# Kernel tuning notes

Measured on AMD Instinct MI355X. Metric: run time of the kernel, lower is better.

Reference implementation:

```python
import jax, jax.numpy as jnp
import numpy as np
from jax import lax

DIM = 512


def rmsnorm(x, gamma):
    # F.normalize(x, dim=-1) * sqrt(dim) * (gamma + 1)
    n = jnp.maximum(jnp.linalg.norm(x, axis=-1, keepdims=True), 1e-12)
    return x / n * (DIM ** 0.5) * (gamma + 1.0)


def lru_layer(x, Wn, Wif, Whf, bhf):
    # x: [b, t, d]. Precompute the input-dependent projections as big matmuls,
    # then scan the genuinely sequential hidden recurrence.
    nh = jnp.tanh(jnp.einsum('btd,de->bte', x, Wn))   # candidate hidden
    ifg = jnp.einsum('btd,de->bte', x, Wif)            # input forget logits
    b = x.shape[0]
    h0 = jnp.zeros((b, DIM), dtype=x.dtype)            # init_hidden buffer (zeros)

    def step(h, inp):
        nh_t, if_t = inp                               # [b, d] each
        g = jax.nn.sigmoid(h @ Whf + bhf + if_t)       # forget gate
        h_next = h + g * (nh_t - h)                    # lerp(h, nh, g)
        return h_next, h_next

    _, hs = lax.scan(step, h0, (jnp.swapaxes(nh, 0, 1), jnp.swapaxes(ifg, 0, 1)))
    return jnp.swapaxes(hs, 0, 1)                      # [b, t, d]


def gate_cell(x, hidden, Wn, Wif, Whf, bhf):
    # LightRecurrentUnitCell applied pointwise over [b, t, d] with hidden=x_in
    nh = jnp.tanh(jnp.einsum('btd,de->bte', x, Wn))
    g = jax.nn.sigmoid(jnp.einsum('btd,de->bte', hidden, Whf) + bhf
                       + jnp.einsum('btd,de->bte', x, Wif))
    return hidden + g * (nh - hidden)


def setup_inputs() -> dict:
    key = jax.random.key(0)
    ks = jax.random.split(key, 12)
    s = 1.0 / np.sqrt(DIM)
    def w(k):
        return jax.random.uniform(k, (DIM, DIM), jnp.float32, -s, s)
    inp = {
        'x': jax.random.normal(ks[0], (32, 2048, DIM), jnp.float32),
        'gamma': jnp.zeros((DIM,), jnp.float32),
        'g_Wn': w(ks[1]), 'g_Wif': w(ks[2]), 'g_Whf': w(ks[3]),
        'g_bhf': jax.random.uniform(ks[4], (DIM,), jnp.float32, -s, s),
        'l0_Wn': w(ks[5]), 'l0_Wif': w(ks[6]), 'l0_Whf': w(ks[7]),
        'l0_bhf': jax.random.uniform(ks[8], (DIM,), jnp.float32, -s, s),
        'l1_Wn': w(ks[9]), 'l1_Wif': w(ks[10]), 'l1_Whf': w(ks[11]),
        'l1_bhf': jax.random.uniform(jax.random.fold_in(key, 99), (DIM,), jnp.float32, -s, s),
    }
    return inp


def reference(x, gamma, g_Wn, g_Wif, g_Whf, g_bhf,
              l0_Wn, l0_Wif, l0_Whf, l0_bhf,
              l1_Wn, l1_Wif, l1_Whf, l1_bhf):
    xn = rmsnorm(x, gamma)
    h = lru_layer(xn, l0_Wn, l0_Wif, l0_Whf, l0_bhf)
    h = lru_layer(h, l1_Wn, l1_Wif, l1_Whf, l1_bhf)
    lru_out = gate_cell(h, xn, g_Wn, g_Wif, g_Whf, g_bhf)
    return lru_out + x
```

## Files before the change

kernel.cpp:

```cpp
#include <hip/hip_runtime.h>
#include <stdint.h>

#define D 512
#define BATCH 32
#define TT 2048
#define BT (BATCH*TT)

typedef unsigned short u16;
typedef __attribute__((ext_vector_type(8))) short bf16x8;
typedef __attribute__((ext_vector_type(4))) float f32x4;

__device__ __forceinline__ float bf2f(u16 u){
  union { unsigned int i; float f; } v; v.i = ((unsigned int)u) << 16; return v.f;
}
__device__ __forceinline__ u16 f2bf(float f){
  union { float f; unsigned int i; } v; v.f = f;
  unsigned int r = (v.i + 0x7fffu + ((v.i >> 16) & 1u)) >> 16;
  return (u16)r;
}

__device__ __forceinline__ int dot4i8(int a, int b, int c){
#if __has_builtin(__builtin_amdgcn_sdot4)
  return __builtin_amdgcn_sdot4(a, b, c, false);
#else
  c += (int)(char)(a      ) * (int)(char)(b      );
  c += (int)(char)(a >>  8) * (int)(char)(b >>  8);
  c += (int)(char)(a >> 16) * (int)(char)(b >> 16);
  c += (int)(char)(a >> 24) * (int)(char)(b >> 24);
  return c;
#endif
}

__global__ __launch_bounds__(256) void rmsnorm_k(const float* __restrict__ x,
                                                 const float* __restrict__ gamma,
                                                 u16* __restrict__ xn){
  int row = blockIdx.x;
  int t = threadIdx.x;
  const float* xr = x + (size_t)row * D;
  float v0 = xr[t];
  float v1 = xr[t + 256];
  float s = v0*v0 + v1*v1;
  #pragma unroll
  for (int o = 32; o > 0; o >>= 1) s += __shfl_down(s, o);
  __shared__ float red[4];
  int lane = t & 63, wv = t >> 6;
  if (lane == 0) red[wv] = s;
  __syncthreads();
  float tot = red[0] + red[1] + red[2] + red[3];
  float n = fmaxf(sqrtf(tot), 1e-12f);
  float sc = 22.627416997969522f / n;
  u16* o_ = xn + (size_t)row * D;
  o_[t]       = f2bf(v0 * sc * (gamma[t] + 1.f));
  o_[t + 256] = f2bf(v1 * sc * (gamma[t + 256] + 1.f));
}

__global__ __launch_bounds__(256) void transpose_k(const float* __restrict__ src,
                                                   u16* __restrict__ dst){
  __shared__ u16 tile[32][33];
  int bx = blockIdx.x * 32, by = blockIdx.y * 32;
  int tx = threadIdx.x & 31, ty = threadIdx.x >> 5;
  #pragma unroll
  for (int i = 0; i < 32; i += 8)
    tile[ty + i][tx] = f2bf(src[(size_t)(by + ty + i) * D + bx + tx]);
  __syncthreads();
  #pragma unroll
  for (int i = 0; i < 32; i += 8)
    dst[(size_t)(bx + ty + i) * D + by + tx] = tile[tx][ty + i];
}

__global__ __launch_bounds__(64) void quant_col_k(const float* __restrict__ W,
                                                  int* __restrict__ Wq,
                                                  float* __restrict__ sc){
  int e = blockIdx.x;
  int lane = threadIdx.x;
  float w[8];
  float m = 0.f;
  #pragma unroll
  for (int j = 0; j < 8; j++){
    w[j] = W[(size_t)(lane*8 + j) * D + e];
    m = fmaxf(m, fabsf(w[j]));
  }
  #pragma unroll
  for (int o = 32; o > 0; o >>= 1) m = fmaxf(m, __shfl_xor(m, o));
  float inv = (m > 0.f) ? (127.f / m) : 0.f;
  int q[8];
  #pragma unroll
  for (int j = 0; j < 8; j++){
    int v = __float2int_rn(w[j] * inv);
    v = v < -127 ? -127 : (v > 127 ? 127 : v);
    q[j] = v & 0xff;
  }
  int p0 = q[0] | (q[1] << 8) | (q[2] << 16) | (q[3] << 24);
  int p1 = q[4] | (q[5] << 8) | (q[6] << 16) | (q[7] << 24);
  Wq[e*128 + lane*2]     = p0;
  Wq[e*128 + lane*2 + 1] = p1;
  if (lane == 0) sc[e] = m / (127.f * 127.f);
}

__global__ __launch_bounds__(256) void gemm_bt_k(const u16* __restrict__ A,
                                                 const u16* __restrict__ Bt,
                                                 u16* __restrict__ C,
                                                 int do_tanh){
  __shared__ __align__(16) u16 As[128*32];
  __shared__ __align__(16) u16 Bs[128*32];
  int tid = threadIdx.x;
  int bm = blockIdx.x, bn = blockIdx.y;
  int wv = tid >> 6, lane = tid & 63;
  int wm = (wv & 1) * 64, wn = (wv >> 1) * 64;
  int m0 = lane & 15, quad = lane >> 4;
  f32x4 acc[4][4];
  #pragma unroll
  for (int i = 0; i < 4; i++)
    #pragma unroll
    for (int j = 0; j < 4; j++){
      f32x4 z = {0.f, 0.f, 0.f, 0.f};
      acc[i][j] = z;
    }
  const size_t arow = (size_t)bm * 128;
  const size_t brow = (size_t)bn * 128;
  for (int k0 = 0; k0 < D; k0 += 32){
    __syncthreads();
    #pragma unroll
    for (int i = 0; i < 2; i++){
      int c = tid + 256*i;
      int r = c >> 2, ko = (c & 3) * 8;
      ((int4*)As)[c] = *(const int4*)(A  + (arow + r) * D + k0 + ko);
      ((int4*)Bs)[c] = *(const int4*)(Bt + (brow + r) * D + k0 + ko);
    }
    __syncthreads();
    bf16x8 af[4], bfr[4];
    #pragma unroll
    for (int i = 0; i < 4; i++){
      af[i]  = *(const bf16x8*)(As + (wm + i*16 + m0) * 32 + quad*8);
      bfr[i] = *(const bf16x8*)(Bs + (wn + i*16 + m0) * 32 + quad*8);
    }
    #pragma unroll
    for (int i = 0; i < 4; i++)
      #pragma unroll
      for (int j = 0; j < 4; j++)
        acc[i][j] = __builtin_amdgcn_mfma_f32_16x16x32_bf16(af[i], bfr[j], acc[i][j], 0, 0, 0);
  }
  #pragma unroll
  for (int i = 0; i < 4; i++)
    #pragma unroll
    for (int j = 0; j < 4; j++)
      #pragma unroll
      for (int r = 0; r < 4; r++){
        size_t row = arow + wm + i*16 + quad*4 + r;
        int col = bn*128 + wn + j*16 + m0;
        float v = acc[i][j][r];
        if (do_tanh) v = tanhf(v);
        C[row * D + col] = f2bf(v);
      }
}

__global__ __launch_bounds__(512, 2) void lru_scan_k(u16* __restrict__ Nn,
                                                     const u16* __restrict__ Ff,
                                                     const int* __restrict__ Wq,
                                                     const float* __restrict__ sc,
                                                     const float* __restrict__ bhf){
  int e = threadIdx.x;
  int b = blockIdx.x;
  int w[128];
  #pragma unroll
  for (int i = 0; i < 128; i++) w[i] = Wq[e*128 + i];
  float scale = sc[e];
  float bias  = bhf[e];
  __shared__ __align__(16) int hq[2][128];
  if (e < 128) hq[0][e] = 0;
  float h = 0.f;
  const size_t base = (size_t)b * TT * D + e;
  u16* np = Nn + base;
  const u16* fp = Ff + base;
  float nv = bf2f(np[0]);
  float fv = bf2f(fp[0]);
  __syncthreads();
  for (int t = 0; t < TT; t++){
    float nv_n = 0.f, fv_n = 0.f;
    if (t < TT - 1){
      nv_n = bf2f(np[(size_t)(t+1) * D]);
      fv_n = bf2f(fp[(size_t)(t+1) * D]);
    }
    const int* hb = hq[t & 1];
    int z = 0;
    #pragma unroll
    for (int i = 0; i < 32; i++){
      int4 hc = ((const int4*)hb)[i];
      z = dot4i8(w[4*i+0], hc.x, z);
      z = dot4i8(w[4*i+1], hc.y, z);
      z = dot4i8(w[4*i+2], hc.z, z);
      z = dot4i8(w[4*i+3], hc.w, z);
    }
    float arg = (float)z * scale + bias + fv;
    float g = 1.f / (1.f + __expf(-arg));
    h = h + g * (nv - h);
    np[(size_t)t * D] = f2bf(h);
    int q = __float2int_rn(h * 127.f);
    q = q < -127 ? -127 : (q > 127 ? 127 : q);
    ((char*)hq[(t+1) & 1])[e] = (char)q;
    nv = nv_n; fv = fv_n;
    __syncthreads();
  }
}

__global__ __launch_bounds__(256) void final1_k(const u16* __restrict__ xn,
                                                u16* __restrict__ Nng,
                                                const u16* __restrict__ Ffg,
                                                const u16* __restrict__ Ghf,
                                                const float* __restrict__ gbhf){
  size_t i = (size_t)blockIdx.x * 256 + threadIdx.x;
  int e = (int)(i & (D - 1));
  float xnv = bf2f(xn[i]);
  float nv  = bf2f(Nng[i]);
  float arg = bf2f(Ghf[i]) + gbhf[e] + bf2f(Ffg[i]);
  float g = 1.f / (1.f + __expf(-arg));
  float lru = xnv + g * (nv - xnv);
  Nng[i] = f2bf(lru);
}

__global__ __launch_bounds__(256) void final2_k(const u16* __restrict__ lru,
                                                const float* __restrict__ x,
                                                float* __restrict__ out){
  size_t i = (size_t)blockIdx.x * 256 + threadIdx.x;
  out[i] = bf2f(lru[i]) + x[i];
}

extern "C" void kernel_launch(void* const* d_in, const int* in_sizes, int n_in,
                              void* d_out, int out_size, void* d_ws, size_t ws_size,
                              hipStream_t stream){
  const float* x      = (const float*)d_in[0];
  const float* gamma  = (const float*)d_in[1];
  const float* g_Wn   = (const float*)d_in[2];
  const float* g_Wif  = (const float*)d_in[3];
  const float* g_Whf  = (const float*)d_in[4];
  const float* g_bhf  = (const float*)d_in[5];
  const float* l0_Wn  = (const float*)d_in[6];
  const float* l0_Wif = (const float*)d_in[7];
  const float* l0_Whf = (const float*)d_in[8];
  const float* l0_bhf = (const float*)d_in[9];
  const float* l1_Wn  = (const float*)d_in[10];
  const float* l1_Wif = (const float*)d_in[11];
  const float* l1_Whf = (const float*)d_in[12];
  const float* l1_bhf = (const float*)d_in[13];
  float* out = (float*)d_out;

  char* ws = (char*)d_ws;
  const size_t PLANE = (size_t)BT * D * 2;
  u16* P0 = (u16*)(ws);
  u16* P1 = (u16*)(ws + PLANE);
  u16* P2 = (u16*)d_out;
  u16* P3 = P2 + (size_t)BT * D;

  char* wb = ws + 2*PLANE;
  const size_t WSZ = (size_t)D * D * 2;
  u16* T_l0Wn  = (u16*)(wb + 0*WSZ);
  u16* T_l0Wif = (u16*)(wb + 1*WSZ);
  u16* T_gWhf  = (u16*)(wb + 2*WSZ);
  u16* T_l1Wn  = (u16*)(wb + 3*WSZ);
  u16* T_l1Wif = (u16*)(wb + 4*WSZ);
  u16* T_gWn   = (u16*)(wb + 5*WSZ);
  u16* T_gWif  = (u16*)(wb + 6*WSZ);
  int*   Wq0 = (int*)  (wb + 7*WSZ);
  int*   Wq1 = (int*)  (wb + 7*WSZ + (size_t)D*D);
  float* sc0 = (float*)(wb + 7*WSZ + 2*(size_t)D*D);
  float* sc1 = (float*)(wb + 7*WSZ + 2*(size_t)D*D + D*4);

  dim3 tb(256), tg(16, 16);
  transpose_k<<<tg, tb, 0, stream>>>(l0_Wn,  T_l0Wn);
  transpose_k<<<tg, tb, 0, stream>>>(l0_Wif, T_l0Wif);
  transpose_k<<<tg, tb, 0, stream>>>(g_Whf,  T_gWhf);
  transpose_k<<<tg, tb, 0, stream>>>(l1_Wn,  T_l1Wn);
  transpose_k<<<tg, tb, 0, stream>>>(l1_Wif, T_l1Wif);
  transpose_k<<<tg, tb, 0, stream>>>(g_Wn,   T_gWn);
  transpose_k<<<tg, tb, 0, stream>>>(g_Wif,  T_gWif);
  quant_col_k<<<512, 64, 0, stream>>>(l0_Whf, Wq0, sc0);
  quant_col_k<<<512, 64, 0, stream>>>(l1_Whf, Wq1, sc1);

  rmsnorm_k<<<BT, 256, 0, stream>>>(x, gamma, P0);

  dim3 gg(BT/128, D/128);
  gemm_bt_k<<<gg, tb, 0, stream>>>(P0, T_l0Wn,  P1, 1);
  gemm_bt_k<<<gg, tb, 0, stream>>>(P0, T_l0Wif, P2, 0);
  lru_scan_k<<<BATCH, 512, 0, stream>>>(P1, P2, Wq0, sc0, l0_bhf);
  gemm_bt_k<<<gg, tb, 0, stream>>>(P1, T_l1Wn,  P3, 1);
  gemm_bt_k<<<gg, tb, 0, stream>>>(P1, T_l1Wif, P2, 0);
  lru_scan_k<<<BATCH, 512, 0, stream>>>(P3, P2, Wq1, sc1, l1_bhf);
  gemm_bt_k<<<gg, tb, 0, stream>>>(P3, T_gWn,  P1, 1);
  gemm_bt_k<<<gg, tb, 0, stream>>>(P3, T_gWif, P2, 0);
  gemm_bt_k<<<gg, tb, 0, stream>>>(P0, T_gWhf, P3, 0);

  final1_k<<<BT*D/256, 256, 0, stream>>>(P0, P1, P2, P3, g_bhf);
  final2_k<<<BT*D/256, 256, 0, stream>>>(P1, x, out);
}
```

Baseline: 4.231 ms.

## Split scan dot product between LDS reads and readlane broadcasts with four accumulators

In the LRU scan kernel, each thread now reads the first half of the quantized hidden vector from shared memory as before. For the second half it loads one word per lane and broadcasts it with readlane, which moves part of the traffic off LDS onto scalar registers. The dot product is split across four independent accumulators to shorten the dependency chain, and the bias is folded into the prefetched forget-gate value. Launch bounds drop to one block per SM to leave room for registers. This lowers occupancy, which may hide less latency across batches.

```diff
diff --git a/kernel.cpp b/kernel.cpp
--- a/kernel.cpp
+++ b/kernel.cpp
@@ -28,6 +28,14 @@
   c += (int)(char)(a >> 16) * (int)(char)(b >> 16);
   c += (int)(char)(a >> 24) * (int)(char)(b >> 24);
   return c;
+#endif
+}
+
+__device__ __forceinline__ int rdlane(int v, int l){
+#if __has_builtin(__builtin_amdgcn_readlane)
+  return __builtin_amdgcn_readlane(v, l);
+#else
+  return __shfl(v, l);
 #endif
 }
 
@@ -154,16 +162,19 @@
       }
 }
 
-__global__ __launch_bounds__(512, 2) void lru_scan_k(u16* __restrict__ Nn,
+__global__ __launch_bounds__(512, 1) void lru_scan_k(u16* __restrict__ Nn,
                                                      const u16* __restrict__ Ff,
                                                      const int* __restrict__ Wq,
                                                      const float* __restrict__ sc,
                                                      const float* __restrict__ bhf){
   int e = threadIdx.x;
   int b = blockIdx.x;
-  int w[128];
-  #pragma unroll
-  for (int i = 0; i < 128; i++) w[i] = Wq[e*128 + i];
+  int lane64 = e & 63;
+  int w[64], w2[64];
+  #pragma unroll
+  for (int i = 0; i < 64; i++) w[i]  = Wq[e*128 + i];
+  #pragma unroll
+  for (int i = 0; i < 64; i++) w2[i] = Wq[e*128 + 64 + i];
   float scale = sc[e];
   float bias  = bhf[e];
   __shared__ __align__(16) int hq[2][128];
@@ -172,33 +183,40 @@
   const size_t base = (size_t)b * TT * D + e;
   u16* np = Nn + base;
   const u16* fp = Ff + base;
-  float nv = bf2f(np[0]);
-  float fv = bf2f(fp[0]);
+  float nv  = bf2f(np[0]);
+  float fvb = bf2f(fp[0]) + bias;
   __syncthreads();
   for (int t = 0; t < TT; t++){
-    float nv_n = 0.f, fv_n = 0.f;
+    float nv_n = 0.f, fvb_n = 0.f;
     if (t < TT - 1){
-      nv_n = bf2f(np[(size_t)(t+1) * D]);
-      fv_n = bf2f(fp[(size_t)(t+1) * D]);
+      nv_n  = bf2f(np[(size_t)(t+1) * D]);
+      fvb_n = bf2f(fp[(size_t)(t+1) * D]) + bias;
     }
     const int* hb = hq[t & 1];
-    int z = 0;
-    #pragma unroll
-    for (int i = 0; i < 32; i++){
+    int hrl = hb[64 + lane64];
+    int zz[4] = {0, 0, 0, 0};
+    #pragma unroll
+    for (int i = 0; i < 16; i++){
       int4 hc = ((const int4*)hb)[i];
-      z = dot4i8(w[4*i+0], hc.x, z);
-      z = dot4i8(w[4*i+1], hc.y, z);
-      z = dot4i8(w[4*i+2], hc.z, z);
-      z = dot4i8(w[4*i+3], hc.w, z);
-    }
-    float arg = (float)z * scale + bias + fv;
+      zz[0] = dot4i8(w[4*i+0], hc.x, zz[0]);
+      zz[1] = dot4i8(w[4*i+1], hc.y, zz[1]);
+      zz[2] = dot4i8(w[4*i+2], hc.z, zz[2]);
+      zz[3] = dot4i8(w[4*i+3], hc.w, zz[3]);
+    }
+    #pragma unroll
+    for (int m = 0; m < 64; m++){
+      int s = rdlane(hrl, m);
+      zz[m & 3] = dot4i8(w2[m], s, zz[m & 3]);
+    }
+    int z = (zz[0] + zz[1]) + (zz[2] + zz[3]);
+    float arg = (float)z * scale + fvb;
     float g = 1.f / (1.f + __expf(-arg));
     h = h + g * (nv - h);
     np[(size_t)t * D] = f2bf(h);
     int q = __float2int_rn(h * 127.f);
     q = q < -127 ? -127 : (q > 127 ? 127 : q);
     ((char*)hq[(t+1) & 1])[e] = (char)q;
-    nv = nv_n; fv = fv_n;
+    nv = nv_n; fvb = fvb_n;
     __syncthreads();
   }
 }
```

New measurement: 4.696 ms. +11.0%, slower.

## Use int8 MFMA for the recurrent matvec in the LRU scan kernel

Applied to the files above, without the earlier changes.

Replaces the per-thread sdot4 loop over 128 packed weight registers with 16x16x64 int8 MFMA instructions. Each wave holds its 64 output columns as B fragments and broadcasts the quantized hidden state as the A operand. Only row 0 of each accumulator is used, so most of the MFMA work is wasted, but the per-thread dependent dot chain becomes a few matrix ops. It also folds the bias into the prefetched forget-gate input and swaps __syncthreads for a raw waitcnt plus s_barrier.

```diff
diff --git a/kernel.cpp b/kernel.cpp
--- a/kernel.cpp
+++ b/kernel.cpp
@@ -9,6 +9,7 @@
 typedef unsigned short u16;
 typedef __attribute__((ext_vector_type(8))) short bf16x8;
 typedef __attribute__((ext_vector_type(4))) float f32x4;
+typedef __attribute__((ext_vector_type(4))) int i32x4;
 
 __device__ __forceinline__ float bf2f(u16 u){
   union { unsigned int i; float f; } v; v.i = ((unsigned int)u) << 16; return v.f;
@@ -17,18 +18,6 @@
   union { float f; unsigned int i; } v; v.f = f;
   unsigned int r = (v.i + 0x7fffu + ((v.i >> 16) & 1u)) >> 16;
   return (u16)r;
-}
-
-__device__ __forceinline__ int dot4i8(int a, int b, int c){
-#if __has_builtin(__builtin_amdgcn_sdot4)
-  return __builtin_amdgcn_sdot4(a, b, c, false);
-#else
-  c += (int)(char)(a      ) * (int)(char)(b      );
-  c += (int)(char)(a >>  8) * (int)(char)(b >>  8);
-  c += (int)(char)(a >> 16) * (int)(char)(b >> 16);
-  c += (int)(char)(a >> 24) * (int)(char)(b >> 24);
-  return c;
-#endif
 }
 
 __global__ __launch_bounds__(256) void rmsnorm_k(const float* __restrict__ x,
@@ -159,47 +148,61 @@
                                                      const int* __restrict__ Wq,
                                                      const float* __restrict__ sc,
                                                      const float* __restrict__ bhf){
-  int e = threadIdx.x;
+  int tid = threadIdx.x;
   int b = blockIdx.x;
-  int w[128];
-  #pragma unroll
-  for (int i = 0; i < 128; i++) w[i] = Wq[e*128 + i];
+  int wv  = tid >> 6;
+  int l   = tid & 63;
+  int grp = l >> 4;
+  int col = l & 15;
+  int e   = wv * 64 + l;
+
+  i32x4 bf[4][8];
+  #pragma unroll
+  for (int j = 0; j < 4; j++){
+    const int* wp = Wq + (wv*64 + j*16 + col) * 128;
+    #pragma unroll
+    for (int c = 0; c < 8; c++)
+      bf[j][c] = *(const i32x4*)(wp + c*16 + grp*4);
+  }
   float scale = sc[e];
   float bias  = bhf[e];
-  __shared__ __align__(16) int hq[2][128];
-  if (e < 128) hq[0][e] = 0;
+
+  __shared__ __align__(16) char hq[2][512];
+  if (tid < 128) ((int*)hq[0])[tid] = 0;
   float h = 0.f;
   const size_t base = (size_t)b * TT * D + e;
   u16* np = Nn + base;
   const u16* fp = Ff + base;
-  float nv = bf2f(np[0]);
-  float fv = bf2f(fp[0]);
+  float nv  = bf2f(np[0]);
+  float fvb = bf2f(fp[0]) + bias;
   __syncthreads();
+
   for (int t = 0; t < TT; t++){
-    float nv_n = 0.f, fv_n = 0.f;
+    float nv_n = 0.f, fvb_n = 0.f;
     if (t < TT - 1){
-      nv_n = bf2f(np[(size_t)(t+1) * D]);
-      fv_n = bf2f(fp[(size_t)(t+1) * D]);
-    }
-    const int* hb = hq[t & 1];
-    int z = 0;
-    #pragma unroll
-    for (int i = 0; i < 32; i++){
-      int4 hc = ((const int4*)hb)[i];
-      z = dot4i8(w[4*i+0], hc.x, z);
-      z = dot4i8(w[4*i+1], hc.y, z);
-      z = dot4i8(w[4*i+2], hc.z, z);
-      z = dot4i8(w[4*i+3], hc.w, z);
-    }
-    float arg = (float)z * scale + bias + fv;
+      nv_n  = bf2f(np[(size_t)(t+1) * D]);
+      fvb_n = bf2f(fp[(size_t)(t+1) * D]) + bias;
+    }
+    const char* hb = hq[t & 1];
+    i32x4 acc0 = {0,0,0,0}, acc1 = {0,0,0,0}, acc2 = {0,0,0,0}, acc3 = {0,0,0,0};
+    #pragma unroll
+    for (int c = 0; c < 8; c++){
+      i32x4 a = *(const i32x4*)(hb + c*64 + grp*16);
+      acc0 = __builtin_amdgcn_mfma_i32_16x16x64_i8(a, bf[0][c], acc0, 0, 0, 0);
+      acc1 = __builtin_amdgcn_mfma_i32_16x16x64_i8(a, bf[1][c], acc1, 0, 0, 0);
+      acc2 = __builtin_amdgcn_mfma_i32_16x16x64_i8(a, bf[2][c], acc2, 0, 0, 0);
+      acc3 = __builtin_amdgcn_mfma_i32_16x16x64_i8(a, bf[3][c], acc3, 0, 0, 0);
+    }
+    int z = (grp == 0) ? acc0[0] : (grp == 1) ? acc1[0] : (grp == 2) ? acc2[0] : acc3[0];
+    float arg = (float)z * scale + fvb;
     float g = 1.f / (1.f + __expf(-arg));
     h = h + g * (nv - h);
     np[(size_t)t * D] = f2bf(h);
     int q = __float2int_rn(h * 127.f);
     q = q < -127 ? -127 : (q > 127 ? 127 : q);
-    ((char*)hq[(t+1) & 1])[e] = (char)q;
-    nv = nv_n; fv = fv_n;
-    __syncthreads();
+    hq[(t+1) & 1][e] = (char)q;
+    nv = nv_n; fvb = fvb_n;
+    asm volatile("s_waitcnt lgkmcnt(0)\n\ts_barrier" ::: "memory");
   }
 }
 
```

Result: slower. 4.999 ms (+18.2%).
